# Kernel optimization log

Measured on AMD Instinct MI355X. Metric: run time of the kernel, lower is better.

Reference implementation:

```python
import jax, jax.numpy as jnp
import numpy as np

E = 8
DIMS = [512, 1024, 1024, 512]
BATCH = 2048


def _init_w(key, shape):
    a = np.sqrt(6.0 / (shape[-2] * shape[-1]))
    return jax.random.uniform(key, shape, dtype=jnp.float32, minval=-a, maxval=a)


def setup_inputs() -> dict:
    key = jax.random.key(0)
    ks = jax.random.split(key, 8)
    inp = {
        "weight_blend": jax.random.uniform(ks[0], (BATCH, E), dtype=jnp.float32),
        "x": jax.random.normal(ks[1], (BATCH, DIMS[0]), dtype=jnp.float32),
    }
    for i in range(3):
        inp[f"W{i}"] = _init_w(ks[2 + i], (E, DIMS[i + 1], DIMS[i]))
        inp[f"B{i}"] = jnp.zeros((E, DIMS[i + 1], 1), dtype=jnp.float32)
    return inp


def reference(weight_blend, x, W0, B0, W1, B1, W2, B2):
    Ws = [W0, W1, W2]
    Bs = [B0, B1, B2]
    acts = [jax.nn.elu, jax.nn.elu, None]
    for W, B, act in zip(Ws, Bs, acts):
        # dropout p=0 -> identity
        # blended-expert GEMM: sum_e wb[b,e] * (W[e] @ x[b]) == einsum
        t = jnp.einsum("be,eoi,bi->bo", weight_blend, W, x)
        bias = jnp.einsum("be,eo->bo", weight_blend, B[..., 0])
        x = t + bias
        if act is not None:
            x = act(x)
    return x
```

## Files before the change

### kernel.cpp

```cpp
#include <hip/hip_runtime.h>
#include <math.h>

typedef __attribute__((ext_vector_type(8))) short bf16x8;
typedef __attribute__((ext_vector_type(4))) float f32x4;

#define NEXP 8
#define BATCH 2048

__device__ __forceinline__ unsigned short f2bf(float f) {
    union { float f; unsigned u; } v; v.f = f;
    unsigned r = v.u + 0x7FFFu + ((v.u >> 16) & 1u);
    return (unsigned short)(r >> 16);
}

__device__ __forceinline__ float elu_fast(float v) {
    return v > 0.f ? v : (exp2f(v * 1.4426950408889634f) - 1.0f);
}

__global__ __launch_bounds__(256) void pack_all(
    const float* __restrict__ W0, const float* __restrict__ W1,
    const float* __restrict__ W2, const float* __restrict__ x,
    unsigned short* __restrict__ W0p, unsigned short* __restrict__ W1p,
    unsigned short* __restrict__ W2p, unsigned short* __restrict__ x0p)
{
    __shared__ float T[128 * 36];
    const int bid = blockIdx.x, t = threadIdx.x;

    if (bid < 10240) {
        const float* W; unsigned short* out; int KB, Din, Dout, U, lin;
        if (bid < 2048)      { W = W0; out = W0p; KB = 16; Din = 512;  Dout = 1024; U = 4; lin = bid; }
        else if (bid < 6144) { W = W1; out = W1p; KB = 32; Din = 1024; Dout = 1024; U = 4; lin = bid - 2048; }
        else                 { W = W2; out = W2p; KB = 32; Din = 1024; Dout = 512;  U = 2; lin = bid - 6144; }
        const int e  = lin & 7;
        const int r  = lin >> 3;
        const int kb = r % KB;
        const int nb = r / KB;
        const int N0 = nb * 16 * U;
        const int K0 = kb * 32;
        for (int it = 0; it < U / 2; ++it) {
            const int idx = t + 256 * it;
            const int nl = idx >> 3, k4 = (idx & 7) * 4;
            float4 v = *(const float4*)(W + ((size_t)e * Dout + N0 + nl) * Din + K0 + k4);
            *(float4*)(T + nl * 36 + k4) = v;
        }
        __syncthreads();
        if (t < 64 * U) {
            const int u = t >> 6, l = t & 63;
            const float* p = T + (u * 16 + (l & 15)) * 36 + (l >> 4) * 8;
            bf16x8 h;
            #pragma unroll
            for (int j = 0; j < 8; ++j) h[j] = (short)f2bf(p[j]);
            *(bf16x8*)(out + (size_t)lin * (U * 512) + t * 8) = h;
        }
    } else {
        const int lin = bid - 10240;
        const int kb = lin & 15, mb = lin >> 4;
        for (int it = 0; it < 4; ++it) {
            const int idx = t + 256 * it;
            const int ml = idx >> 3, k4 = (idx & 7) * 4;
            float4 v = *(const float4*)(x + (size_t)(mb * 128 + ml) * 512 + kb * 32 + k4);
            *(float4*)(T + ml * 36 + k4) = v;
        }
        __syncthreads();
        #pragma unroll
        for (int it = 0; it < 2; ++it) {
            const int s = t + 256 * it;
            const int g = s >> 6, l = s & 63;
            const float* p = T + (g * 16 + (l & 15)) * 36 + (l >> 4) * 8;
            bf16x8 h;
            #pragma unroll
            for (int j = 0; j < 8; ++j) h[j] = (short)f2bf(p[j]);
            *(bf16x8*)(x0p + (size_t)lin * 4096 + s * 8) = h;
        }
    }
}

template<int UP>
__device__ __forceinline__ void moe_body64(
    float* lds_f,
    const unsigned short* __restrict__ Xp,
    const unsigned short* __restrict__ Wp,
    const float* __restrict__ Bias,
    const float* __restrict__ WBl,
    void* __restrict__ Yout,
    int KB, int Dout, int KBn, int act, int packed_out)
{
    constexpr int PSTR = 68;

    const int tid  = threadIdx.x;
    const int ew   = tid >> 6;
    const int l    = tid & 63;
    const int lh   = l >> 4;
    const int ll   = l & 15;
    const int e0   = 2 * ew;
    const int bx   = blockIdx.x;
    const int by   = blockIdx.y;
    const int m0   = by * 64;
    const int n0   = bx * 64;
    const int mb   = by >> 1;
    const int half = by & 1;

    f32x4 acc0[4][4], acc1[4][4];
    #pragma unroll
    for (int t = 0; t < 4; ++t)
        #pragma unroll
        for (int u = 0; u < 4; ++u)
            #pragma unroll
            for (int i = 0; i < 4; ++i) { acc0[t][u][i] = 0.f; acc1[t][u][i] = 0.f; }

    unsigned aoff[4];
    #pragma unroll
    for (int t = 0; t < 4; ++t)
        aoff[t] = (unsigned)(mb * KB) * 8192u + (unsigned)(half * 4 + t) * 1024u + l * 16u;
    unsigned boff0[4], boff1[4];
    #pragma unroll
    for (int u = 0; u < 4; ++u) {
        const int fn = bx * 4 + u;
        const int nb = fn / UP;
        const int uu = fn % UP;
        boff0[u] = (((unsigned)(nb * KB) * 8 + e0) * UP + uu) * 1024u + l * 16u;
        boff1[u] = boff0[u] + UP * 1024u;
    }
    const unsigned astr = 8192u;
    const unsigned bstr = UP * 8192u;
    const char* xc = (const char*)Xp;
    const char* wc = (const char*)Wp;

    bf16x8 aR[2][4], b0R[2][4], b1R[2][4];

    auto LOAD = [&](int s, int kk) {
        const unsigned ab = (unsigned)kk * astr;
        const unsigned bb = (unsigned)kk * bstr;
        #pragma unroll
        for (int t = 0; t < 4; ++t)
            aR[s][t] = *(const bf16x8*)(xc + aoff[t] + ab);
        #pragma unroll
        for (int u = 0; u < 4; ++u) {
            b0R[s][u] = *(const bf16x8*)(wc + boff0[u] + bb);
            b1R[s][u] = *(const bf16x8*)(wc + boff1[u] + bb);
        }
    };
    auto MF = [&](int s) {
        #pragma unroll
        for (int u = 0; u < 4; ++u)
            #pragma unroll
            for (int t = 0; t < 4; ++t) {
                acc0[t][u] = __builtin_amdgcn_mfma_f32_16x16x32_bf16(aR[s][t], b0R[s][u], acc0[t][u], 0, 0, 0);
                acc1[t][u] = __builtin_amdgcn_mfma_f32_16x16x32_bf16(aR[s][t], b1R[s][u], acc1[t][u], 0, 0, 0);
            }
    };

    LOAD(0, 0);
    for (int kk = 0; kk < KB; kk += 2) {
        if (kk + 1 < KB) LOAD(1, kk + 1);
        MF(0);
        if (kk + 2 < KB) LOAD(0, kk + 2);
        MF(1);
    }

    float bi0[4], bi1[4];
    #pragma unroll
    for (int u = 0; u < 4; ++u) {
        const int n = n0 + u * 16 + ll;
        bi0[u] = Bias[(size_t)e0 * Dout + n];
        bi1[u] = Bias[(size_t)(e0 + 1) * Dout + n];
    }
    float2 wbp[4][4];
    #pragma unroll
    for (int t = 0; t < 4; ++t)
        #pragma unroll
        for (int r = 0; r < 4; ++r) {
            const int lm = 16 * t + 4 * lh + r;
            wbp[t][r] = ((const float2*)(WBl + (size_t)(m0 + lm) * NEXP))[ew];
        }

    float* pb = lds_f + ew * (64 * PSTR);
    #pragma unroll
    for (int t = 0; t < 4; ++t)
        #pragma unroll
        for (int r = 0; r < 4; ++r) {
            const int lm = 16 * t + 4 * lh + r;
            #pragma unroll
            for (int u = 0; u < 4; ++u)
                pb[lm * PSTR + u * 16 + ll] =
                    wbp[t][r].x * (acc0[t][u][r] + bi0[u]) + wbp[t][r].y * (acc1[t][u][r] + bi1[u]);
        }
    __syncthreads();

    if (packed_out) {
        #pragma unroll
        for (int it = 0; it < 2; ++it) {
            const int kbh = it;
            const int g   = tid >> 6;
            const int le  = tid & 63;
            const int lhh = le >> 4, lle = le & 15;
            const int rb  = (g * 16 + lle) * PSTR + kbh * 32 + lhh * 8;
            bf16x8 h;
            #pragma unroll
            for (int j = 0; j < 8; ++j) {
                float v = lds_f[0 * 64 * PSTR + rb + j]
                        + lds_f[1 * 64 * PSTR + rb + j]
                        + lds_f[2 * 64 * PSTR + rb + j]
                        + lds_f[3 * 64 * PSTR + rb + j];
                if (act) v = elu_fast(v);
                h[j] = (short)f2bf(v);
            }
            unsigned short* dst = (unsigned short*)Yout +
                ((size_t)(mb * KBn + bx * 2 + kbh) * 8 + half * 4 + g) * 512 + le * 8;
            *(bf16x8*)dst = h;
        }
    } else {
        #pragma unroll
        for (int it = 0; it < 4; ++it) {
            const int idx = tid + 256 * it;
            const int row = idx >> 4;
            const int c4  = (idx & 15) * 4;
            const int rb  = row * PSTR + c4;
            float4 s  = *(const float4*)(lds_f + 0 * 64 * PSTR + rb);
            float4 q1 = *(const float4*)(lds_f + 1 * 64 * PSTR + rb);
            float4 q2 = *(const float4*)(lds_f + 2 * 64 * PSTR + rb);
            float4 q3 = *(const float4*)(lds_f + 3 * 64 * PSTR + rb);
            s.x += q1.x + q2.x + q3.x;
            s.y += q1.y + q2.y + q3.y;
            s.z += q1.z + q2.z + q3.z;
            s.w += q1.w + q2.w + q3.w;
            if (act) {
                s.x = elu_fast(s.x);
                s.y = elu_fast(s.y);
                s.z = elu_fast(s.z);
                s.w = elu_fast(s.w);
            }
            *(float4*)((float*)Yout + (size_t)(m0 + row) * Dout + n0 + c4) = s;
        }
    }
}

__global__ __launch_bounds__(256, 2) void moe_l0(
    const unsigned short* __restrict__ Xp, const unsigned short* __restrict__ Wp,
    const float* __restrict__ Bias, const float* __restrict__ WBl,
    void* __restrict__ Yout, int KB, int Dout, int KBn, int act, int packed_out)
{
    __shared__ __align__(16) float lds_f[4 * 64 * 68];
    moe_body64<4>(lds_f, Xp, Wp, Bias, WBl, Yout, KB, Dout, KBn, act, packed_out);
}
__global__ __launch_bounds__(256, 2) void moe_l1(
    const unsigned short* __restrict__ Xp, const unsigned short* __restrict__ Wp,
    const float* __restrict__ Bias, const float* __restrict__ WBl,
    void* __restrict__ Yout, int KB, int Dout, int KBn, int act, int packed_out)
{
    __shared__ __align__(16) float lds_f[4 * 64 * 68];
    moe_body64<4>(lds_f, Xp, Wp, Bias, WBl, Yout, KB, Dout, KBn, act, packed_out);
}
__global__ __launch_bounds__(256, 2) void moe_l2(
    const unsigned short* __restrict__ Xp, const unsigned short* __restrict__ Wp,
    const float* __restrict__ Bias, const float* __restrict__ WBl,
    void* __restrict__ Yout, int KB, int Dout, int KBn, int act, int packed_out)
{
    __shared__ __align__(16) float lds_f[4 * 64 * 68];
    moe_body64<2>(lds_f, Xp, Wp, Bias, WBl, Yout, KB, Dout, KBn, act, packed_out);
}

#define BM 64
#define BNF 64
#define BKF 16
#define PAD 4

__global__ __launch_bounds__(256) void moe_layer_f32(
    const float* __restrict__ X, const float* __restrict__ W,
    const float* __restrict__ Bias, const float* __restrict__ WB,
    float* __restrict__ Y, int Din, int Dout, int act)
{
    __shared__ float As[BKF][BM + PAD];
    __shared__ float Bs[BKF][BNF + PAD];
    const int tid = threadIdx.x;
    const int tm = tid >> 4, tn = tid & 15;
    const int m0 = blockIdx.y * BM, n0 = blockIdx.x * BNF;
    const int lr = tid >> 2, lc = (tid & 3) << 2;
    float acc[4][4] = {};
    const float* xrow  = X  + (size_t)(m0 + lr) * Din;
    const float* wbrow = WB + (size_t)(m0 + lr) * NEXP;
    const float* wrow0 = W  + (size_t)(n0 + lr) * Din;
    for (int e = 0; e < NEXP; ++e) {
        const float wbe = wbrow[e];
        const float* wrow = wrow0 + (size_t)e * Dout * Din;
        for (int k0 = 0; k0 < Din; k0 += BKF) {
            float4 av = *(const float4*)(xrow + k0 + lc);
            float4 bv = *(const float4*)(wrow + k0 + lc);
            __syncthreads();
            As[lc+0][lr] = av.x*wbe; As[lc+1][lr] = av.y*wbe;
            As[lc+2][lr] = av.z*wbe; As[lc+3][lr] = av.w*wbe;
            Bs[lc+0][lr] = bv.x; Bs[lc+1][lr] = bv.y;
            Bs[lc+2][lr] = bv.z; Bs[lc+3][lr] = bv.w;
            __syncthreads();
            #pragma unroll
            for (int k = 0; k < BKF; ++k) {
                float4 a = *(const float4*)&As[k][tm << 2];
                float4 b = *(const float4*)&Bs[k][tn << 2];
                acc[0][0]+=a.x*b.x; acc[0][1]+=a.x*b.y; acc[0][2]+=a.x*b.z; acc[0][3]+=a.x*b.w;
                acc[1][0]+=a.y*b.x; acc[1][1]+=a.y*b.y; acc[1][2]+=a.y*b.z; acc[1][3]+=a.y*b.w;
                acc[2][0]+=a.z*b.x; acc[2][1]+=a.z*b.y; acc[2][2]+=a.z*b.z; acc[2][3]+=a.z*b.w;
                acc[3][0]+=a.w*b.x; acc[3][1]+=a.w*b.y; acc[3][2]+=a.w*b.z; acc[3][3]+=a.w*b.w;
            }
        }
    }
    #pragma unroll
    for (int im = 0; im < 4; ++im) {
        const int m = m0 + (tm << 2) + im;
        const float* wbm = WB + (size_t)m * NEXP;
        float wv[NEXP];
        #pragma unroll
        for (int e = 0; e < NEXP; ++e) wv[e] = wbm[e];
        #pragma unroll
        for (int in = 0; in < 4; ++in) {
            const int n = n0 + (tn << 2) + in;
            float bsum = 0.f;
            #pragma unroll
            for (int e = 0; e < NEXP; ++e) bsum += wv[e] * Bias[(size_t)e * Dout + n];
            float v = acc[im][in] + bsum;
            if (act) v = v > 0.f ? v : expm1f(v);
            acc[im][in] = v;
        }
        float4 o = make_float4(acc[im][0], acc[im][1], acc[im][2], acc[im][3]);
        *(float4*)(Y + (size_t)m * Dout + n0 + (tn << 2)) = o;
    }
}

extern "C" void kernel_launch(void* const* d_in, const int* in_sizes, int n_in,
                              void* d_out, int out_size, void* d_ws, size_t ws_size,
                              hipStream_t stream)
{
    (void)in_sizes; (void)n_in; (void)out_size;
    const float* wb = (const float*)d_in[0];
    const float* x  = (const float*)d_in[1];
    const float* W0 = (const float*)d_in[2];
    const float* B0 = (const float*)d_in[3];
    const float* W1 = (const float*)d_in[4];
    const float* B1 = (const float*)d_in[5];
    const float* W2 = (const float*)d_in[6];
    const float* B2 = (const float*)d_in[7];
    float* out = (float*)d_out;

    const size_t NW0 = (size_t)8*1024*512, NW1 = (size_t)8*1024*1024, NW2 = (size_t)8*512*1024;
    const size_t NX0 = (size_t)BATCH*512, NX1 = (size_t)BATCH*1024;
    const size_t need = (NW0 + NW1 + NW2 + NX0 + 2 * NX1) * 2;

    if (ws_size >= need) {
        unsigned short* W0p = (unsigned short*)d_ws;
        unsigned short* W1p = W0p + NW0;
        unsigned short* W2p = W1p + NW1;
        unsigned short* x0p = W2p + NW2;
        unsigned short* x1p = x0p + NX0;
        unsigned short* x2p = x1p + NX1;
        pack_all<<<10496, 256, 0, stream>>>(W0, W1, W2, x, W0p, W1p, W2p, x0p);
        moe_l0<<<dim3(16, 32), 256, 0, stream>>>(x0p, W0p, B0, wb, x1p, 16, 1024, 32, 1, 1);
        moe_l1<<<dim3(16, 32), 256, 0, stream>>>(x1p, W1p, B1, wb, x2p, 32, 1024, 32, 1, 1);
        moe_l2<<<dim3(8, 32),  256, 0, stream>>>(x2p, W2p, B2, wb, out, 32, 512,  0, 0, 0);
    } else {
        float* x1 = (float*)d_ws;
        float* x2 = x1 + (size_t)BATCH * 1024;
        moe_layer_f32<<<dim3(1024/BNF, BATCH/BM), 256, 0, stream>>>(x,  W0, B0, wb, x1, 512,  1024, 1);
        moe_layer_f32<<<dim3(1024/BNF, BATCH/BM), 256, 0, stream>>>(x1, W1, B1, wb, x2, 1024, 1024, 1);
        moe_layer_f32<<<dim3(512/BNF,  BATCH/BM), 256, 0, stream>>>(x2, W2, B2, wb, out, 1024, 512,  0);
    }
}
```

Baseline: 195.2 us.

## Fuse layers 0 and 1 into one persistent kernel with grid barrier

Merges the first two MoE layer launches into one kernel that runs layer 0, waits on an atomic counter-based grid-wide barrier, then runs layer 1. The barrier counter is reset inside the pack kernel. It also raises wave priority around the MFMA block. This removes one kernel launch and its tail drain, but it relies on all 512 blocks being co-resident. If occupancy (2 blocks/CU) does not fit all blocks, the kernel can deadlock, and the spin-wait adds its own cost.

Result: slower. 325.1 us (+66.6%).

```diff
diff --git a/kernel.cpp b/kernel.cpp
--- a/kernel.cpp
+++ b/kernel.cpp
@@ -21,10 +21,12 @@
     const float* __restrict__ W0, const float* __restrict__ W1,
     const float* __restrict__ W2, const float* __restrict__ x,
     unsigned short* __restrict__ W0p, unsigned short* __restrict__ W1p,
-    unsigned short* __restrict__ W2p, unsigned short* __restrict__ x0p)
+    unsigned short* __restrict__ W2p, unsigned short* __restrict__ x0p,
+    unsigned* __restrict__ bar)
 {
     __shared__ float T[128 * 36];
     const int bid = blockIdx.x, t = threadIdx.x;
+    if (bid == 0 && t == 0) *bar = 0u;
 
     if (bid < 10240) {
         const float* W; unsigned short* out; int KB, Din, Dout, U, lin;
@@ -141,6 +143,7 @@
         }
     };
     auto MF = [&](int s) {
+        __builtin_amdgcn_s_setprio(1);
         #pragma unroll
         for (int u = 0; u < 4; ++u)
             #pragma unroll
@@ -148,6 +151,7 @@
                 acc0[t][u] = __builtin_amdgcn_mfma_f32_16x16x32_bf16(aR[s][t], b0R[s][u], acc0[t][u], 0, 0, 0);
                 acc1[t][u] = __builtin_amdgcn_mfma_f32_16x16x32_bf16(aR[s][t], b1R[s][u], acc1[t][u], 0, 0, 0);
             }
+        __builtin_amdgcn_s_setprio(0);
     };
 
     LOAD(0, 0);
@@ -235,22 +239,33 @@
     }
 }
 
-__global__ __launch_bounds__(256, 2) void moe_l0(
-    const unsigned short* __restrict__ Xp, const unsigned short* __restrict__ Wp,
-    const float* __restrict__ Bias, const float* __restrict__ WBl,
-    void* __restrict__ Yout, int KB, int Dout, int KBn, int act, int packed_out)
+__global__ __launch_bounds__(256, 2) void moe_l01(
+    const unsigned short* __restrict__ x0p, const unsigned short* __restrict__ W0p,
+    const float* __restrict__ B0,
+    unsigned short* __restrict__ x1p,
+    const unsigned short* __restrict__ W1p, const float* __restrict__ B1,
+    const float* __restrict__ WBl,
+    unsigned short* __restrict__ x2p,
+    unsigned* __restrict__ bar)
 {
     __shared__ __align__(16) float lds_f[4 * 64 * 68];
-    moe_body64<4>(lds_f, Xp, Wp, Bias, WBl, Yout, KB, Dout, KBn, act, packed_out);
-}
-__global__ __launch_bounds__(256, 2) void moe_l1(
-    const unsigned short* __restrict__ Xp, const unsigned short* __restrict__ Wp,
-    const float* __restrict__ Bias, const float* __restrict__ WBl,
-    void* __restrict__ Yout, int KB, int Dout, int KBn, int act, int packed_out)
-{
-    __shared__ __align__(16) float lds_f[4 * 64 * 68];
-    moe_body64<4>(lds_f, Xp, Wp, Bias, WBl, Yout, KB, Dout, KBn, act, packed_out);
-}
+
+    moe_body64<4>(lds_f, x0p, W0p, B0, WBl, (void*)x1p, 16, 1024, 32, 1, 1);
+
+    const unsigned nblk = gridDim.x * gridDim.y;
+    __syncthreads();
+    __threadfence();
+    if (threadIdx.x == 0) {
+        atomicAdd(bar, 1u);
+        while (__hip_atomic_load(bar, __ATOMIC_ACQUIRE, __HIP_MEMORY_SCOPE_AGENT) < nblk)
+            __builtin_amdgcn_s_sleep(8);
+    }
+    __syncthreads();
+    __threadfence();
+
+    moe_body64<4>(lds_f, x1p, W1p, B1, WBl, (void*)x2p, 32, 1024, 32, 1, 1);
+}
+
 __global__ __launch_bounds__(256, 2) void moe_l2(
     const unsigned short* __restrict__ Xp, const unsigned short* __restrict__ Wp,
     const float* __restrict__ Bias, const float* __restrict__ WBl,
@@ -342,7 +357,7 @@
 
     const size_t NW0 = (size_t)8*1024*512, NW1 = (size_t)8*1024*1024, NW2 = (size_t)8*512*1024;
     const size_t NX0 = (size_t)BATCH*512, NX1 = (size_t)BATCH*1024;
-    const size_t need = (NW0 + NW1 + NW2 + NX0 + 2 * NX1) * 2;
+    const size_t need = (NW0 + NW1 + NW2 + NX0 + 2 * NX1) * 2 + 64;
 
     if (ws_size >= need) {
         unsigned short* W0p = (unsigned short*)d_ws;
@@ -351,9 +366,9 @@
         unsigned short* x0p = W2p + NW2;
         unsigned short* x1p = x0p + NX0;
         unsigned short* x2p = x1p + NX1;
-        pack_all<<<10496, 256, 0, stream>>>(W0, W1, W2, x, W0p, W1p, W2p, x0p);
-        moe_l0<<<dim3(16, 32), 256, 0, stream>>>(x0p, W0p, B0, wb, x1p, 16, 1024, 32, 1, 1);
-        moe_l1<<<dim3(16, 32), 256, 0, stream>>>(x1p, W1p, B1, wb, x2p, 32, 1024, 32, 1, 1);
+        unsigned* bar = (unsigned*)(x2p + NX1);
+        pack_all<<<10496, 256, 0, stream>>>(W0, W1, W2, x, W0p, W1p, W2p, x0p, bar);
+        moe_l01<<<dim3(16, 32), 256, 0, stream>>>(x0p, W0p, B0, x1p, W1p, B1, wb, x2p, bar);
         moe_l2<<<dim3(8, 32),  256, 0, stream>>>(x2p, W2p, B2, wb, out, 32, 512,  0, 0, 0);
     } else {
         float* x1 = (float*)d_ws;
```
